# Optimization experiments

Hardware: AMD Instinct MI355X
Metric: run time of the kernel (lower is better)

Reference implementation:

```python
import jax, jax.numpy as jnp
import numpy as np

B, HW, ENC, E, D, A, V, L = 64, 14, 2048, 512, 512, 512, 32000, 32
LN_EPS = 1e-5


def setup_inputs() -> dict:
    key = jax.random.key(0)
    ks = jax.random.split(key, 16)
    s = 0.02
    n = lambda k, sh: jax.random.normal(k, sh, jnp.float32)
    encoder_out = n(ks[0], (B, HW, HW, ENC))
    encoded_captions = jax.random.randint(ks[1], (B, L), 0, V)
    caption_lengths = jax.random.randint(ks[2], (B, 1), 2, L + 1)
    caption_lengths = caption_lengths.at[0, 0].set(L)  # ensure max length present
    return dict(
        encoder_out=encoder_out,
        encoded_captions=encoded_captions,
        caption_lengths=caption_lengths,
        emb=n(ks[3], (V, E)) * s,
        W_enc_att=n(ks[4], (A, ENC)) * s, b_enc_att=jnp.zeros((A,)),
        W_dec_att=n(ks[5], (A, D)) * s, b_dec_att=jnp.zeros((A,)),
        W_full_att=n(ks[6], (1, A)) * s, b_full_att=jnp.zeros((1,)),
        W_ih=n(ks[7], (4 * D, E + ENC)) * s, b_ih=jnp.zeros((4 * D,)),
        W_hh=n(ks[8], (4 * D, D)) * s, b_hh=jnp.zeros((4 * D,)),
        g_h=jnp.ones((D,)), be_h=jnp.zeros((D,)),
        g_c=jnp.ones((D,)), be_c=jnp.zeros((D,)),
        W_init_h=n(ks[9], (D, ENC)) * s, b_init_h=jnp.zeros((D,)),
        W_init_c=n(ks[10], (D, ENC)) * s, b_init_c=jnp.zeros((D,)),
        W_beta=n(ks[11], (ENC, D)) * s, b_beta=jnp.zeros((ENC,)),
        W_fc=n(ks[12], (V, D)) * s, b_fc=jnp.zeros((V,)),
    )


def _layer_norm(x, g, b):
    m = x.mean(-1, keepdims=True)
    v = ((x - m) ** 2).mean(-1, keepdims=True)
    return (x - m) / jnp.sqrt(v + LN_EPS) * g + b


def reference(encoder_out, encoded_captions, caption_lengths, emb,
              W_enc_att, b_enc_att, W_dec_att, b_dec_att, W_full_att, b_full_att,
              W_ih, b_ih, W_hh, b_hh, g_h, be_h, g_c, be_c,
              W_init_h, b_init_h, W_init_c, b_init_c, W_beta, b_beta, W_fc, b_fc):
    bsz = encoder_out.shape[0]
    enc_out = encoder_out.reshape(bsz, -1, encoder_out.shape[-1])  # [B,P,ENC]
    lengths = caption_lengths[:, 0]
    order = jnp.argsort(-lengths)  # stable descending sort (matches torch sort)
    lengths = lengths[order]
    enc_out = enc_out[order]
    caps = encoded_captions[order]
    embeds = emb[caps]  # [B,L,E]
    decode_lengths = lengths - 1
    T = caps.shape[1] - 1  # static max(decode_lengths)

    mean_enc = enc_out.mean(axis=1)
    h = _layer_norm(mean_enc @ W_init_h.T + b_init_h, g_h, be_h)
    c = _layer_norm(mean_enc @ W_init_c.T + b_init_c, g_c, be_c)

    att1 = enc_out @ W_enc_att.T + b_enc_att  # [B,P,A] precomputed once
    prev_seq = jnp.swapaxes(embeds[:, :T], 0, 1)  # [T,B,E] teacher-forced inputs
    masks = jnp.arange(T)[:, None] < decode_lengths[None, :]  # [T,B] active rows

    def step(carry, xs):
        h, c = carry
        prev, mask = xs
        # attention
        att2 = h @ W_dec_att.T + b_dec_att  # [B,A]
        e = jax.nn.relu(att1 + att2[:, None, :]) @ W_full_att[0] + b_full_att[0]  # [B,P]
        alpha = jax.nn.softmax(e, axis=1)
        awe = jnp.einsum('bpe,bp->be', enc_out, alpha)  # [B,ENC]
        gate = jax.nn.sigmoid(h @ W_beta.T + b_beta)
        awe = gate * awe
        # LSTM cell
        x = jnp.concatenate([prev, awe], axis=1)  # [B,E+ENC]
        gates = x @ W_ih.T + b_ih + h @ W_hh.T + b_hh
        i, f, g, o = jnp.split(gates, 4, axis=1)
        c_new = jax.nn.sigmoid(f) * c + jax.nn.sigmoid(i) * jnp.tanh(g)
        h_new = jax.nn.sigmoid(o) * jnp.tanh(c_new)
        h_new = _layer_norm(h_new, g_h, be_h)
        c_new = _layer_norm(c_new, g_c, be_c)
        preds = h_new @ W_fc.T + b_fc  # [B,V]; dropout is identity in eval
        m = mask[:, None]
        h = jnp.where(m, h_new, h)  # freeze finished rows (== torch batch shrink)
        c = jnp.where(m, c_new, c)
        return (h, c), (jnp.where(m, preds, 0.0), jnp.where(m, alpha, 0.0))

    (_, _), (preds_t, alphas_t) = jax.lax.scan(step, (h, c), (prev_seq, masks))
    predictions = jnp.swapaxes(preds_t, 0, 1)  # [B,T,V]
    alphas = jnp.swapaxes(alphas_t, 0, 1)      # [B,T,P]
    return predictions, caps, decode_lengths, alphas, order
```

## Files before the change

### kernel.cpp

```cpp
#include <hip/hip_runtime.h>
#include <cfloat>
#include <math.h>

#define B_ 64
#define P_ 196
#define ENC_ 2048
#define D_ 512
#define V_ 32000
#define L_ 32
#define T_ 31

#define OUT_PREDS 0L
#define OUT_CAPS  63488000L
#define OUT_DECL  63490048L
#define OUT_ALPH  63490112L
#define OUT_ORDER 63878976L

typedef __bf16 bf16;
typedef __bf16 bf16x8 __attribute__((ext_vector_type(8)));
typedef __bf16 bf16x4 __attribute__((ext_vector_type(4)));
typedef __bf16 bf16x2 __attribute__((ext_vector_type(2)));
typedef float  f32x4  __attribute__((ext_vector_type(4)));

static __device__ __forceinline__ float sigmoidf_(float x) { return 1.f / (1.f + __expf(-x)); }

__global__ void k_order(const int* __restrict__ cap_len, const int* __restrict__ caps,
                        int* __restrict__ order_i, int* __restrict__ declen_i,
                        int* __restrict__ caps_i, float* __restrict__ out)
{
    __shared__ int len_s[B_];
    int tid = threadIdx.x;
    len_s[tid] = cap_len[tid];
    __syncthreads();
    int li = len_s[tid];
    int pos = 0;
    for (int j = 0; j < B_; ++j) {
        int lj = len_s[j];
        pos += (lj > li) || (lj == li && j < tid);
    }
    order_i[pos]  = tid;
    declen_i[pos] = li - 1;
    out[OUT_ORDER + pos] = (float)tid;
    out[OUT_DECL  + pos] = (float)(li - 1);
    for (int l = 0; l < L_; ++l) {
        int tok = caps[tid * L_ + l];
        caps_i[pos * L_ + l] = tok;
        out[OUT_CAPS + pos * L_ + l] = (float)tok;
    }
}

__global__ __launch_bounds__(256) void k_cvt(const float* __restrict__ in, bf16* __restrict__ ob, long n)
{
    long i = ((long)blockIdx.x * 256 + threadIdx.x) * 8;
    if (i >= n) return;
    float4 a = *(const float4*)(in + i);
    float4 b = *(const float4*)(in + i + 4);
    bf16x8 v;
    v[0]=(bf16)a.x; v[1]=(bf16)a.y; v[2]=(bf16)a.z; v[3]=(bf16)a.w;
    v[4]=(bf16)b.x; v[5]=(bf16)b.y; v[6]=(bf16)b.z; v[7]=(bf16)b.w;
    *(bf16x8*)(ob + i) = v;
}

__global__ __launch_bounds__(256) void k_cvt_enc(const float* __restrict__ enc,
                                                 const int* __restrict__ order_i,
                                                 bf16* __restrict__ enc_s)
{
    long i = ((long)blockIdx.x * 256 + threadIdx.x) * 8;
    int b = (int)(i / ((long)P_ * ENC_));
    long rem = i - (long)b * P_ * ENC_;
    const float* src = enc + (long)order_i[b] * P_ * ENC_ + rem;
    float4 a = *(const float4*)(src);
    float4 c = *(const float4*)(src + 4);
    bf16x8 v;
    v[0]=(bf16)a.x; v[1]=(bf16)a.y; v[2]=(bf16)a.z; v[3]=(bf16)a.w;
    v[4]=(bf16)c.x; v[5]=(bf16)c.y; v[6]=(bf16)c.z; v[7]=(bf16)c.w;
    *(bf16x8*)(enc_s + i) = v;
}

__global__ __launch_bounds__(256) void k_meanb(const bf16* __restrict__ enc_s, bf16* __restrict__ mean_b)
{
    int b = blockIdx.x, col = blockIdx.y * 256 + threadIdx.x;
    float s = 0.f;
    const bf16* eb = enc_s + (long)b * P_ * ENC_ + col;
    for (int p = 0; p < P_; ++p) s += (float)eb[(long)p * ENC_];
    mean_b[(long)b * ENC_ + col] = (bf16)(s * (1.f / (float)P_));
}

template<int FUSE, int EPI, int SWZ>
__global__ void __launch_bounds__(256)
k_mgemm(const bf16* __restrict__ A, long lda,
        const bf16* __restrict__ B1, const bf16* __restrict__ B2,
        const float* __restrict__ bias,
        float* __restrict__ Cf, bf16* __restrict__ Cb,
        int N, int K, int kspl, int Nsp, int Ksp,
        const int* __restrict__ declen_i)
{
    const int tid = threadIdx.x;
    const int lane = tid & 63, w = tid >> 6;
    int mt, nt, z;
    if (SWZ == 0)      { mt = blockIdx.x; nt = blockIdx.y; z = blockIdx.z; }
    else if (SWZ == 1) { int o = blockIdx.x; int wg = (o & 7) * 98 + (o >> 3);
                         mt = wg >> 2; nt = wg & 3; z = 0; }
    else               { int o = blockIdx.x; int xcd = o & 7;
                         int base = xcd < 6 ? xcd * 969 : 5814 + (xcd - 6) * 968;
                         int wg = base + (o >> 3);
                         nt = wg / 31; mt = wg - 31 * nt; z = 0; }
    const int krange = K / kspl;
    const int k0 = z * krange, k1 = k0 + krange;
    const int r16 = lane & 15, kq = lane >> 4;
    const int koff = kq * 8;

    const bf16* Ap = A + (long)(mt * 64 + r16) * lda + koff;
    const int ncol0 = nt * 128 + w * 32;

    const bf16* Bp[2];
    const bf16* B2p[2];
#pragma unroll
    for (int ni = 0; ni < 2; ++ni) {
        int n = ncol0 + ni * 16 + r16;
        if (FUSE == 1)
            Bp[ni] = (n < Nsp) ? B1 + (long)n * K + koff
                               : B2 + (long)(n - Nsp) * K + koff;
        else if (FUSE == 2) {
            Bp[ni]  = B1 + (long)n * Ksp + koff;
            B2p[ni] = B2 + (long)n * (K - Ksp) + koff - Ksp;
        } else
            Bp[ni] = B1 + (long)n * K + koff;
    }

    auto loadA = [&](int kk, bf16x8* dst) {
#pragma unroll
        for (int mi = 0; mi < 4; ++mi)
            dst[mi] = *(const bf16x8*)(Ap + (long)mi * 16 * lda + kk);
    };
    auto loadB = [&](int kk, bf16x8* dst) {
#pragma unroll
        for (int ni = 0; ni < 2; ++ni) {
            if (FUSE == 2 && kk >= Ksp) dst[ni] = *(const bf16x8*)(B2p[ni] + kk);
            else                        dst[ni] = *(const bf16x8*)(Bp[ni] + kk);
        }
    };

    f32x4 acc[4][2] = {};
    bf16x8 af[4], bfr[2];
    loadA(k0, af); loadB(k0, bfr);
    for (int kk = k0 + 32; kk < k1; kk += 32) {
        bf16x8 af2[4], bf2[2];
        loadA(kk, af2); loadB(kk, bf2);
#pragma unroll
        for (int mi = 0; mi < 4; ++mi)
#pragma unroll
            for (int ni = 0; ni < 2; ++ni)
                acc[mi][ni] = __builtin_amdgcn_mfma_f32_16x16x32_bf16(bfr[ni], af[mi], acc[mi][ni], 0, 0, 0);
#pragma unroll
        for (int mi = 0; mi < 4; ++mi) af[mi] = af2[mi];
#pragma unroll
        for (int ni = 0; ni < 2; ++ni) bfr[ni] = bf2[ni];
    }
#pragma unroll
    for (int mi = 0; mi < 4; ++mi)
#pragma unroll
        for (int ni = 0; ni < 2; ++ni)
            acc[mi][ni] = __builtin_amdgcn_mfma_f32_16x16x32_bf16(bfr[ni], af[mi], acc[mi][ni], 0, 0, 0);

#pragma unroll
    for (int mi = 0; mi < 4; ++mi) {
        const int row = mt * 64 + mi * 16 + r16;
#pragma unroll
        for (int ni = 0; ni < 2; ++ni) {
            const int col = ncol0 + ni * 16 + kq * 4;
            f32x4 v = acc[mi][ni];
            if (EPI == 0) {
                *(f32x4*)(Cf + (long)z * 64 * N + (long)row * N + col) = v;
            } else if (EPI == 1) {
                f32x4 bv = *(const f32x4*)(bias + col);
                bf16x4 o;
                o[0]=(bf16)(v[0]+bv[0]); o[1]=(bf16)(v[1]+bv[1]);
                o[2]=(bf16)(v[2]+bv[2]); o[3]=(bf16)(v[3]+bv[3]);
                *(bf16x4*)(Cb + (long)row * N + col) = o;
            } else {
                int tt = row >> 6, b = row & 63;
                bool msk = tt < declen_i[b];
                f32x4 bv = *(const f32x4*)(bias + col);
                f32x4 o;
                o[0] = msk ? v[0]+bv[0] : 0.f; o[1] = msk ? v[1]+bv[1] : 0.f;
                o[2] = msk ? v[2]+bv[2] : 0.f; o[3] = msk ? v[3]+bv[3] : 0.f;
                *(f32x4*)(Cf + OUT_PREDS + ((long)b * T_ + tt) * V_ + col) = o;
            }
        }
    }
}

static __device__ __forceinline__ void ln_stats(float x, float* r1, float* r2,
                                                float& m, float& var)
{
    int tid = threadIdx.x;
    r1[tid] = x; r2[tid] = x * x;
    __syncthreads();
    for (int s = 256; s > 0; s >>= 1) {
        if (tid < s) { r1[tid] += r1[tid + s]; r2[tid] += r2[tid + s]; }
        __syncthreads();
    }
    m = r1[0] * (1.f / 512.f);
    var = r2[0] * (1.f / 512.f) - m * m;
    __syncthreads();
}

__global__ __launch_bounds__(512)
void k_initln(const float* __restrict__ pi,
              const float* __restrict__ b_h, const float* __restrict__ b_c,
              const float* __restrict__ g_h, const float* __restrict__ be_h,
              const float* __restrict__ g_c, const float* __restrict__ be_c,
              bf16* __restrict__ xh, float* __restrict__ c)
{
    int b = blockIdx.x, d = threadIdx.x;
    float yh = pi[(long)b * 1024 + d]       + b_h[d];
    float yc = pi[(long)b * 1024 + 512 + d] + b_c[d];
    __shared__ float r1[512], r2[512];
    float m, v;
    ln_stats(yh, r1, r2, m, v);
    xh[(long)b * 3072 + 2560 + d] = (bf16)((yh - m) * rsqrtf(v + 1e-5f) * g_h[d] + be_h[d]);
    ln_stats(yc, r1, r2, m, v);
    c[(long)b * 512 + d] = (yc - m) * rsqrtf(v + 1e-5f) * g_c[d] + be_c[d];
}

__global__ __launch_bounds__(256)
void k_alpha(const float* __restrict__ att2gate, const float* __restrict__ b_dec,
             const float* __restrict__ Wfull, const bf16* __restrict__ att1_b,
             const int* __restrict__ caps_i, const int* __restrict__ declen_i,
             const float* __restrict__ emb, float* __restrict__ alpha_b,
             bf16* __restrict__ xh, float* __restrict__ out, int t)
{
    const int b = blockIdx.x, tid = threadIdx.x;
    if (t >= declen_i[b]) {
        if (tid < P_) out[OUT_ALPH + ((long)b * T_ + t) * P_ + tid] = 0.f;
        return;
    }
    __shared__ float att2s[512], wf[512], red[256];
    for (int i = tid; i < 512; i += 256) {
        float s = b_dec[i];
#pragma unroll
        for (int zz = 0; zz < 4; ++zz) s += att2gate[((long)zz * 64 + b) * 2560 + i];
        att2s[i] = s;
        wf[i] = Wfull[i];
    }
    __syncthreads();
    float ev = -FLT_MAX;
    if (tid < P_) {
        const bf16* ar = att1_b + ((long)b * P_ + tid) * 512;
        float acc = 0.f;
        for (int a0 = 0; a0 < 512; a0 += 8) {
            bf16x8 v = *(const bf16x8*)(ar + a0);
#pragma unroll
            for (int j = 0; j < 8; ++j)
                acc += fmaxf((float)v[j] + att2s[a0 + j], 0.f) * wf[a0 + j];
        }
        ev = acc;
    }
    red[tid] = ev;
    __syncthreads();
    for (int s = 128; s > 0; s >>= 1) { if (tid < s) red[tid] = fmaxf(red[tid], red[tid + s]); __syncthreads(); }
    float mx = red[0];
    __syncthreads();
    float ex = (tid < P_) ? __expf(ev - mx) : 0.f;
    red[tid] = ex;
    __syncthreads();
    for (int s = 128; s > 0; s >>= 1) { if (tid < s) red[tid] += red[tid + s]; __syncthreads(); }
    float inv = 1.f / red[0];
    if (tid < P_) {
        float al = ex * inv;
        alpha_b[b * P_ + tid] = al;
        out[OUT_ALPH + ((long)b * T_ + t) * P_ + tid] = al;
    }
    int tok = caps_i[b * L_ + t];
    for (int i = tid; i < 512; i += 256)
        xh[(long)b * 3072 + i] = (bf16)emb[(long)tok * 512 + i];
}

__global__ __launch_bounds__(256)
void k_awe(const float* __restrict__ alpha_b, const float* __restrict__ att2gate,
           const float* __restrict__ b_beta, const bf16* __restrict__ enc_s,
           const int* __restrict__ declen_i, bf16* __restrict__ xh, int t)
{
    const int b = blockIdx.x, tid = threadIdx.x;
    if (t >= declen_i[b]) return;
    __shared__ float alp[P_];
    if (tid < P_) alp[tid] = alpha_b[b * P_ + tid];
    __syncthreads();
    const int col = blockIdx.y * 512 + tid * 2;
    const bf16* eb = enc_s + (long)b * P_ * ENC_ + col;
    float a0 = 0.f, a1 = 0.f;
#pragma unroll 4
    for (int p = 0; p < P_; ++p) {
        bf16x2 v = *(const bf16x2*)(eb + (long)p * ENC_);
        float al = alp[p];
        a0 += al * (float)v[0]; a1 += al * (float)v[1];
    }
    float g0 = b_beta[col], g1 = b_beta[col + 1];
#pragma unroll
    for (int zz = 0; zz < 4; ++zz) {
        const float* gs = att2gate + ((long)zz * 64 + b) * 2560 + 512 + col;
        g0 += gs[0]; g1 += gs[1];
    }
    bf16x2 o;
    o[0] = (bf16)(a0 * sigmoidf_(g0));
    o[1] = (bf16)(a1 * sigmoidf_(g1));
    *(bf16x2*)(xh + (long)b * 3072 + 512 + col) = o;
}

__global__ __launch_bounds__(512)
void k_lstm(const float* __restrict__ gp, const float* __restrict__ b_ih, const float* __restrict__ b_hh,
            const float* __restrict__ g_h, const float* __restrict__ be_h,
            const float* __restrict__ g_c, const float* __restrict__ be_c,
            bf16* __restrict__ xh, float* __restrict__ c, bf16* __restrict__ hseq,
            const int* __restrict__ declen_i, int t)
{
    int b = blockIdx.x, d = threadIdx.x;
    if (t >= declen_i[b]) return;
    float iv = b_ih[d]        + b_hh[d];
    float fv = b_ih[512 + d]  + b_hh[512 + d];
    float gv = b_ih[1024 + d] + b_hh[1024 + d];
    float ov = b_ih[1536 + d] + b_hh[1536 + d];
    for (int s = 0; s < 8; ++s) {
        const float* gs = gp + ((long)s * B_ + b) * 2048;
        iv += gs[d]; fv += gs[512 + d]; gv += gs[1024 + d]; ov += gs[1536 + d];
    }
    float cn = sigmoidf_(fv) * c[(long)b * 512 + d] + sigmoidf_(iv) * tanhf(gv);
    float hn = sigmoidf_(ov) * tanhf(cn);
    __shared__ float r1[512], r2[512];
    float m, v;
    ln_stats(hn, r1, r2, m, v);
    float hln = (hn - m) * rsqrtf(v + 1e-5f) * g_h[d] + be_h[d];
    ln_stats(cn, r1, r2, m, v);
    float cln = (cn - m) * rsqrtf(v + 1e-5f) * g_c[d] + be_c[d];
    bf16 hv = (bf16)hln;
    xh[(long)b * 3072 + 2560 + d] = hv;
    hseq[((long)t * B_ + b) * 512 + d] = hv;
    c[(long)b * 512 + d] = cln;
}

extern "C" void kernel_launch(void* const* d_in, const int* in_sizes, int n_in,
                              void* d_out, int out_size, void* d_ws, size_t ws_size,
                              hipStream_t stream)
{
    const float* enc       = (const float*)d_in[0];
    const int*   caps      = (const int*)  d_in[1];
    const int*   caplen    = (const int*)  d_in[2];
    const float* emb       = (const float*)d_in[3];
    const float* W_enc_att = (const float*)d_in[4];
    const float* b_enc_att = (const float*)d_in[5];
    const float* W_dec_att = (const float*)d_in[6];
    const float* b_dec_att = (const float*)d_in[7];
    const float* W_full    = (const float*)d_in[8];
    const float* W_ih      = (const float*)d_in[10];
    const float* b_ih      = (const float*)d_in[11];
    const float* W_hh      = (const float*)d_in[12];
    const float* b_hh      = (const float*)d_in[13];
    const float* g_h       = (const float*)d_in[14];
    const float* be_h      = (const float*)d_in[15];
    const float* g_c       = (const float*)d_in[16];
    const float* be_c      = (const float*)d_in[17];
    const float* W_init_h  = (const float*)d_in[18];
    const float* b_init_h  = (const float*)d_in[19];
    const float* W_init_c  = (const float*)d_in[20];
    const float* b_init_c  = (const float*)d_in[21];
    const float* W_beta    = (const float*)d_in[22];
    const float* b_beta    = (const float*)d_in[23];
    const float* W_fc      = (const float*)d_in[24];
    const float* b_fc      = (const float*)d_in[25];
    float* out = (float*)d_out;

    char* w = (char*)d_ws;
    auto alloc = [&](size_t bytes) { char* p = w; w += (bytes + 255) & ~(size_t)255; return p; };
    int*   order_i  = (int*)  alloc(B_ * 4);
    int*   declen_i = (int*)  alloc(B_ * 4);
    int*   caps_i   = (int*)  alloc(B_ * L_ * 4);
    bf16*  enc_s    = (bf16*) alloc((size_t)B_ * P_ * ENC_ * 2);
    bf16*  mean_b   = (bf16*) alloc((size_t)B_ * ENC_ * 2);
    bf16*  att1_b   = (bf16*) alloc((size_t)B_ * P_ * 512 * 2);
    float* pi       = (float*)alloc((size_t)B_ * 1024 * 4);
    float* att2gate = (float*)alloc((size_t)4 * B_ * 2560 * 4);
    float* alpha_b  = (float*)alloc((size_t)B_ * P_ * 4);
    bf16*  xh       = (bf16*) alloc((size_t)B_ * 3072 * 2);
    float* gp       = (float*)alloc((size_t)8 * B_ * 2048 * 4);
    float* cbuf     = (float*)alloc((size_t)B_ * 512 * 4);
    bf16*  hseq     = (bf16*) alloc((size_t)T_ * B_ * 512 * 2);
    bf16*  W_enc_b  = (bf16*) alloc((size_t)512 * 2048 * 2);
    bf16*  W_dec_b  = (bf16*) alloc((size_t)512 * 512 * 2);
    bf16*  W_beta_b = (bf16*) alloc((size_t)2048 * 512 * 2);
    bf16*  W_ih_b   = (bf16*) alloc((size_t)2048 * 2560 * 2);
    bf16*  W_hh_b   = (bf16*) alloc((size_t)2048 * 512 * 2);
    bf16*  W_fc_b   = (bf16*) alloc((size_t)32000 * 512 * 2);
    bf16*  W_inh_b  = (bf16*) alloc((size_t)512 * 2048 * 2);
    bf16*  W_inc_b  = (bf16*) alloc((size_t)512 * 2048 * 2);

    k_order<<<1, B_, 0, stream>>>(caplen, caps, order_i, declen_i, caps_i, out);
    k_cvt_enc<<<12544, 256, 0, stream>>>(enc, order_i, enc_s);
    k_meanb<<<dim3(B_, 8), 256, 0, stream>>>(enc_s, mean_b);

    auto cvt = [&](const float* src, bf16* dst, long n) {
        k_cvt<<<(int)((n / 8 + 255) / 256), 256, 0, stream>>>(src, dst, n);
    };
    cvt(W_enc_att, W_enc_b, 512L * 2048);
    cvt(W_dec_att, W_dec_b, 512L * 512);
    cvt(W_beta,    W_beta_b, 2048L * 512);
    cvt(W_ih,      W_ih_b,  2048L * 2560);
    cvt(W_hh,      W_hh_b,  2048L * 512);
    cvt(W_fc,      W_fc_b,  32000L * 512);
    cvt(W_init_h,  W_inh_b, 512L * 2048);
    cvt(W_init_c,  W_inc_b, 512L * 2048);

    k_mgemm<1, 0, 0><<<dim3(1, 8, 1), 256, 0, stream>>>(mean_b, 2048, W_inh_b, W_inc_b,
        nullptr, pi, nullptr, 1024, 2048, 1, 512, 0, nullptr);
    k_initln<<<B_, 512, 0, stream>>>(pi, b_init_h, b_init_c, g_h, be_h, g_c, be_c, xh, cbuf);

    k_mgemm<0, 1, 1><<<784, 256, 0, stream>>>(enc_s, 2048, W_enc_b, nullptr,
        b_enc_att, nullptr, att1_b, 512, 2048, 1, 0, 0, nullptr);

    for (int t = 0; t < T_; ++t) {
        k_mgemm<1, 0, 0><<<dim3(1, 20, 4), 256, 0, stream>>>(xh + 2560, 3072, W_dec_b, W_beta_b,
            nullptr, att2gate, nullptr, 2560, 512, 4, 512, 0, nullptr);
        k_alpha<<<B_, 256, 0, stream>>>(att2gate, b_dec_att, W_full, att1_b,
            caps_i, declen_i, emb, alpha_b, xh, out, t);
        k_awe<<<dim3(B_, 4), 256, 0, stream>>>(alpha_b, att2gate, b_beta, enc_s,
            declen_i, xh, t);
        k_mgemm<2, 0, 0><<<dim3(1, 16, 8), 256, 0, stream>>>(xh, 3072, W_ih_b, W_hh_b,
            nullptr, gp, nullptr, 2048, 3072, 8, 0, 2560, nullptr);
        k_lstm<<<B_, 512, 0, stream>>>(gp, b_ih, b_hh, g_h, be_h, g_c, be_c,
            xh, cbuf, hseq, declen_i, t);
    }

    k_mgemm<0, 2, 2><<<7750, 256, 0, stream>>>(hseq, 512, W_fc_b, nullptr,
        b_fc, out, nullptr, V_, 512, 1, 0, 0, declen_i);
}
```

Before: 2.516 ms.

## Fuse per-timestep decoder kernels into one persistent kernel with grid barriers

Replaces the 31×5 per-timestep kernel launches (attention GEMM, alpha, awe, LSTM GEMM, LSTM cell) with a single persistent kernel of 256 blocks that loops over timesteps and separates phases with a software global barrier built on atomics. The attention-weighted encoding is now computed by 4 blocks per batch row, and each of those blocks recomputes the softmax redundantly so alpha no longer goes through global memory. The aim is to remove launch overhead and inter-kernel gaps on the serial recurrence. In exchange it relies on all 256 blocks being co-resident and spinning, and each phase leaves many blocks idle.

```diff
diff --git a/kernel.cpp b/kernel.cpp
--- a/kernel.cpp
+++ b/kernel.cpp
@@ -9,6 +9,7 @@
 #define V_ 32000
 #define L_ 32
 #define T_ 31
+#define NBLK_ 256
 
 #define OUT_PREDS 0L
 #define OUT_CAPS  63488000L
@@ -26,10 +27,12 @@
 
 __global__ void k_order(const int* __restrict__ cap_len, const int* __restrict__ caps,
                         int* __restrict__ order_i, int* __restrict__ declen_i,
-                        int* __restrict__ caps_i, float* __restrict__ out)
+                        int* __restrict__ caps_i, float* __restrict__ out,
+                        unsigned* __restrict__ bar)
 {
     __shared__ int len_s[B_];
     int tid = threadIdx.x;
+    if (tid == 0) { bar[0] = 0u; bar[1] = 0u; }
     len_s[tid] = cap_len[tid];
     __syncthreads();
     int li = len_s[tid];
@@ -92,7 +95,7 @@
         const bf16* __restrict__ B1, const bf16* __restrict__ B2,
         const float* __restrict__ bias,
         float* __restrict__ Cf, bf16* __restrict__ Cb,
-        int N, int K, int kspl, int Nsp, int Ksp,
+        int N, int K, int kspl, int Nsp,
         const int* __restrict__ declen_i)
 {
     const int tid = threadIdx.x;
@@ -114,39 +117,28 @@
     const int ncol0 = nt * 128 + w * 32;
 
     const bf16* Bp[2];
-    const bf16* B2p[2];
 #pragma unroll
     for (int ni = 0; ni < 2; ++ni) {
         int n = ncol0 + ni * 16 + r16;
         if (FUSE == 1)
             Bp[ni] = (n < Nsp) ? B1 + (long)n * K + koff
                                : B2 + (long)(n - Nsp) * K + koff;
-        else if (FUSE == 2) {
-            Bp[ni]  = B1 + (long)n * Ksp + koff;
-            B2p[ni] = B2 + (long)n * (K - Ksp) + koff - Ksp;
-        } else
+        else
             Bp[ni] = B1 + (long)n * K + koff;
     }
-
-    auto loadA = [&](int kk, bf16x8* dst) {
-#pragma unroll
-        for (int mi = 0; mi < 4; ++mi)
-            dst[mi] = *(const bf16x8*)(Ap + (long)mi * 16 * lda + kk);
-    };
-    auto loadB = [&](int kk, bf16x8* dst) {
-#pragma unroll
-        for (int ni = 0; ni < 2; ++ni) {
-            if (FUSE == 2 && kk >= Ksp) dst[ni] = *(const bf16x8*)(B2p[ni] + kk);
-            else                        dst[ni] = *(const bf16x8*)(Bp[ni] + kk);
-        }
-    };
 
     f32x4 acc[4][2] = {};
     bf16x8 af[4], bfr[2];
-    loadA(k0, af); loadB(k0, bfr);
+#pragma unroll
+    for (int mi = 0; mi < 4; ++mi) af[mi] = *(const bf16x8*)(Ap + (long)mi * 16 * lda + k0);
+#pragma unroll
+    for (int ni = 0; ni < 2; ++ni) bfr[ni] = *(const bf16x8*)(Bp[ni] + k0);
     for (int kk = k0 + 32; kk < k1; kk += 32) {
         bf16x8 af2[4], bf2[2];
-        loadA(kk, af2); loadB(kk, bf2);
+#pragma unroll
+        for (int mi = 0; mi < 4; ++mi) af2[mi] = *(const bf16x8*)(Ap + (long)mi * 16 * lda + kk);
+#pragma unroll
+        for (int ni = 0; ni < 2; ++ni) bf2[ni] = *(const bf16x8*)(Bp[ni] + kk);
 #pragma unroll
         for (int mi = 0; mi < 4; ++mi)
 #pragma unroll
@@ -224,119 +216,234 @@
     c[(long)b * 512 + d] = (yc - m) * rsqrtf(v + 1e-5f) * g_c[d] + be_c[d];
 }
 
+static __device__ __forceinline__ void gbar(unsigned* bar)
+{
+    __threadfence();
+    __syncthreads();
+    if (threadIdx.x == 0) {
+        unsigned g = __hip_atomic_load(&bar[1], __ATOMIC_RELAXED, __HIP_MEMORY_SCOPE_AGENT);
+        unsigned a = __hip_atomic_fetch_add(&bar[0], 1u, __ATOMIC_ACQ_REL, __HIP_MEMORY_SCOPE_AGENT);
+        if (a == (unsigned)(NBLK_ - 1)) {
+            __hip_atomic_store(&bar[0], 0u, __ATOMIC_RELAXED, __HIP_MEMORY_SCOPE_AGENT);
+            __hip_atomic_store(&bar[1], g + 1u, __ATOMIC_RELEASE, __HIP_MEMORY_SCOPE_AGENT);
+        } else {
+            while (__hip_atomic_load(&bar[1], __ATOMIC_RELAXED, __HIP_MEMORY_SCOPE_AGENT) == g)
+                __builtin_amdgcn_s_sleep(1);
+        }
+    }
+    __syncthreads();
+    __threadfence();
+}
+
 __global__ __launch_bounds__(256)
-void k_alpha(const float* __restrict__ att2gate, const float* __restrict__ b_dec,
-             const float* __restrict__ Wfull, const bf16* __restrict__ att1_b,
+void k_steps(const bf16* __restrict__ att1_b, const bf16* __restrict__ enc_s,
+             const bf16* __restrict__ Wd,  const bf16* __restrict__ Wbt,
+             const bf16* __restrict__ Wih, const bf16* __restrict__ Whh,
+             const float* __restrict__ b_dec, const float* __restrict__ b_beta,
+             const float* __restrict__ Wfull,
+             const float* __restrict__ b_ih, const float* __restrict__ b_hh,
+             const float* __restrict__ g_h, const float* __restrict__ be_h,
+             const float* __restrict__ g_c, const float* __restrict__ be_c,
              const int* __restrict__ caps_i, const int* __restrict__ declen_i,
-             const float* __restrict__ emb, float* __restrict__ alpha_b,
-             bf16* __restrict__ xh, float* __restrict__ out, int t)
-{
-    const int b = blockIdx.x, tid = threadIdx.x;
-    if (t >= declen_i[b]) {
-        if (tid < P_) out[OUT_ALPH + ((long)b * T_ + t) * P_ + tid] = 0.f;
-        return;
-    }
-    __shared__ float att2s[512], wf[512], red[256];
-    for (int i = tid; i < 512; i += 256) {
-        float s = b_dec[i];
-#pragma unroll
-        for (int zz = 0; zz < 4; ++zz) s += att2gate[((long)zz * 64 + b) * 2560 + i];
-        att2s[i] = s;
-        wf[i] = Wfull[i];
-    }
-    __syncthreads();
-    float ev = -FLT_MAX;
-    if (tid < P_) {
-        const bf16* ar = att1_b + ((long)b * P_ + tid) * 512;
-        float acc = 0.f;
-        for (int a0 = 0; a0 < 512; a0 += 8) {
-            bf16x8 v = *(const bf16x8*)(ar + a0);
-#pragma unroll
-            for (int j = 0; j < 8; ++j)
-                acc += fmaxf((float)v[j] + att2s[a0 + j], 0.f) * wf[a0 + j];
+             const float* __restrict__ emb,
+             bf16* __restrict__ xh, float* __restrict__ cst,
+             float* __restrict__ att2gate, float* __restrict__ gp,
+             bf16* __restrict__ hseq, float* __restrict__ out,
+             unsigned* __restrict__ bar)
+{
+    const int bid = blockIdx.x, tid = threadIdx.x;
+    const int lane = tid & 63, w = tid >> 6;
+    const int r16 = lane & 15, kq = lane >> 4, koff = kq * 8;
+    __shared__ float att2s[512], wf[512], red[256], alp[P_];
+    __shared__ float r1[256], r2[256];
+
+    for (int t = 0; t < T_; ++t) {
+        if (bid < 80) {
+            const int nt = bid % 20, z = bid / 20;
+            const int k0 = z * 128;
+            const int ncol0 = nt * 128 + w * 32;
+            const bf16* Ap = xh + 2560 + (long)r16 * 3072 + koff;
+            const bf16* Bp[2];
+#pragma unroll
+            for (int ni = 0; ni < 2; ++ni) {
+                int n = ncol0 + ni * 16 + r16;
+                Bp[ni] = ((n < 512) ? Wd + (long)n * 512 : Wbt + (long)(n - 512) * 512) + koff;
+            }
+            f32x4 acc[4][2] = {};
+#pragma unroll
+            for (int kk = k0; kk < k0 + 128; kk += 32) {
+                bf16x8 af[4], bfr[2];
+#pragma unroll
+                for (int mi = 0; mi < 4; ++mi) af[mi] = *(const bf16x8*)(Ap + (long)mi * 16 * 3072 + kk);
+#pragma unroll
+                for (int ni = 0; ni < 2; ++ni) bfr[ni] = *(const bf16x8*)(Bp[ni] + kk);
+#pragma unroll
+                for (int mi = 0; mi < 4; ++mi)
+#pragma unroll
+                    for (int ni = 0; ni < 2; ++ni)
+                        acc[mi][ni] = __builtin_amdgcn_mfma_f32_16x16x32_bf16(bfr[ni], af[mi], acc[mi][ni], 0, 0, 0);
+            }
+            float* C = att2gate + (long)z * 64 * 2560;
+#pragma unroll
+            for (int mi = 0; mi < 4; ++mi) {
+                const int row = mi * 16 + r16;
+#pragma unroll
+                for (int ni = 0; ni < 2; ++ni)
+                    *(f32x4*)(C + (long)row * 2560 + ncol0 + ni * 16 + kq * 4) = acc[mi][ni];
+            }
         }
-        ev = acc;
-    }
-    red[tid] = ev;
-    __syncthreads();
-    for (int s = 128; s > 0; s >>= 1) { if (tid < s) red[tid] = fmaxf(red[tid], red[tid + s]); __syncthreads(); }
-    float mx = red[0];
-    __syncthreads();
-    float ex = (tid < P_) ? __expf(ev - mx) : 0.f;
-    red[tid] = ex;
-    __syncthreads();
-    for (int s = 128; s > 0; s >>= 1) { if (tid < s) red[tid] += red[tid + s]; __syncthreads(); }
-    float inv = 1.f / red[0];
-    if (tid < P_) {
-        float al = ex * inv;
-        alpha_b[b * P_ + tid] = al;
-        out[OUT_ALPH + ((long)b * T_ + t) * P_ + tid] = al;
-    }
-    int tok = caps_i[b * L_ + t];
-    for (int i = tid; i < 512; i += 256)
-        xh[(long)b * 3072 + i] = (bf16)emb[(long)tok * 512 + i];
-}
-
-__global__ __launch_bounds__(256)
-void k_awe(const float* __restrict__ alpha_b, const float* __restrict__ att2gate,
-           const float* __restrict__ b_beta, const bf16* __restrict__ enc_s,
-           const int* __restrict__ declen_i, bf16* __restrict__ xh, int t)
-{
-    const int b = blockIdx.x, tid = threadIdx.x;
-    if (t >= declen_i[b]) return;
-    __shared__ float alp[P_];
-    if (tid < P_) alp[tid] = alpha_b[b * P_ + tid];
-    __syncthreads();
-    const int col = blockIdx.y * 512 + tid * 2;
-    const bf16* eb = enc_s + (long)b * P_ * ENC_ + col;
-    float a0 = 0.f, a1 = 0.f;
+        gbar(bar);
+
+        {
+            const int b = bid >> 2, seg = bid & 3;
+            if (t < declen_i[b]) {
+                for (int i = tid; i < 512; i += 256) {
+                    float s = b_dec[i];
+#pragma unroll
+                    for (int z = 0; z < 4; ++z) s += att2gate[((long)z * 64 + b) * 2560 + i];
+                    att2s[i] = s;
+                    wf[i] = Wfull[i];
+                }
+                __syncthreads();
+                float ev = -FLT_MAX;
+                if (tid < P_) {
+                    const bf16* ar = att1_b + ((long)b * P_ + tid) * 512;
+                    float acc = 0.f;
+                    for (int a0 = 0; a0 < 512; a0 += 8) {
+                        bf16x8 v = *(const bf16x8*)(ar + a0);
+#pragma unroll
+                        for (int j = 0; j < 8; ++j)
+                            acc += fmaxf((float)v[j] + att2s[a0 + j], 0.f) * wf[a0 + j];
+                    }
+                    ev = acc;
+                }
+                red[tid] = ev;
+                __syncthreads();
+                for (int s = 128; s > 0; s >>= 1) { if (tid < s) red[tid] = fmaxf(red[tid], red[tid + s]); __syncthreads(); }
+                float mx = red[0];
+                __syncthreads();
+                float ex = (tid < P_) ? __expf(ev - mx) : 0.f;
+                red[tid] = ex;
+                __syncthreads();
+                for (int s = 128; s > 0; s >>= 1) { if (tid < s) red[tid] += red[tid + s]; __syncthreads(); }
+                float inv = 1.f / red[0];
+                if (tid < P_) alp[tid] = ex * inv;
+                __syncthreads();
+                if (seg == 1 && tid < P_)
+                    out[OUT_ALPH + ((long)b * T_ + t) * P_ + tid] = alp[tid];
+                const int c0 = seg * 512 + tid * 2;
+                const bf16* eb = enc_s + (long)b * P_ * ENC_ + c0;
+                float a0 = 0.f, a1 = 0.f;
 #pragma unroll 4
-    for (int p = 0; p < P_; ++p) {
-        bf16x2 v = *(const bf16x2*)(eb + (long)p * ENC_);
-        float al = alp[p];
-        a0 += al * (float)v[0]; a1 += al * (float)v[1];
-    }
-    float g0 = b_beta[col], g1 = b_beta[col + 1];
-#pragma unroll
-    for (int zz = 0; zz < 4; ++zz) {
-        const float* gs = att2gate + ((long)zz * 64 + b) * 2560 + 512 + col;
-        g0 += gs[0]; g1 += gs[1];
-    }
-    bf16x2 o;
-    o[0] = (bf16)(a0 * sigmoidf_(g0));
-    o[1] = (bf16)(a1 * sigmoidf_(g1));
-    *(bf16x2*)(xh + (long)b * 3072 + 512 + col) = o;
-}
-
-__global__ __launch_bounds__(512)
-void k_lstm(const float* __restrict__ gp, const float* __restrict__ b_ih, const float* __restrict__ b_hh,
-            const float* __restrict__ g_h, const float* __restrict__ be_h,
-            const float* __restrict__ g_c, const float* __restrict__ be_c,
-            bf16* __restrict__ xh, float* __restrict__ c, bf16* __restrict__ hseq,
-            const int* __restrict__ declen_i, int t)
-{
-    int b = blockIdx.x, d = threadIdx.x;
-    if (t >= declen_i[b]) return;
-    float iv = b_ih[d]        + b_hh[d];
-    float fv = b_ih[512 + d]  + b_hh[512 + d];
-    float gv = b_ih[1024 + d] + b_hh[1024 + d];
-    float ov = b_ih[1536 + d] + b_hh[1536 + d];
-    for (int s = 0; s < 8; ++s) {
-        const float* gs = gp + ((long)s * B_ + b) * 2048;
-        iv += gs[d]; fv += gs[512 + d]; gv += gs[1024 + d]; ov += gs[1536 + d];
-    }
-    float cn = sigmoidf_(fv) * c[(long)b * 512 + d] + sigmoidf_(iv) * tanhf(gv);
-    float hn = sigmoidf_(ov) * tanhf(cn);
-    __shared__ float r1[512], r2[512];
-    float m, v;
-    ln_stats(hn, r1, r2, m, v);
-    float hln = (hn - m) * rsqrtf(v + 1e-5f) * g_h[d] + be_h[d];
-    ln_stats(cn, r1, r2, m, v);
-    float cln = (cn - m) * rsqrtf(v + 1e-5f) * g_c[d] + be_c[d];
-    bf16 hv = (bf16)hln;
-    xh[(long)b * 3072 + 2560 + d] = hv;
-    hseq[((long)t * B_ + b) * 512 + d] = hv;
-    c[(long)b * 512 + d] = cln;
+                for (int p = 0; p < P_; ++p) {
+                    bf16x2 v = *(const bf16x2*)(eb + (long)p * ENC_);
+                    float al = alp[p];
+                    a0 += al * (float)v[0]; a1 += al * (float)v[1];
+                }
+                float g0 = b_beta[c0], g1 = b_beta[c0 + 1];
+#pragma unroll
+                for (int z = 0; z < 4; ++z) {
+                    const float* gs = att2gate + ((long)z * 64 + b) * 2560 + 512 + c0;
+                    g0 += gs[0]; g1 += gs[1];
+                }
+                bf16x2 o;
+                o[0] = (bf16)(a0 * sigmoidf_(g0));
+                o[1] = (bf16)(a1 * sigmoidf_(g1));
+                *(bf16x2*)(xh + (long)b * 3072 + 512 + c0) = o;
+                if (seg == 0) {
+                    int tok = caps_i[b * L_ + t];
+                    for (int i = tid; i < 512; i += 256)
+                        xh[(long)b * 3072 + i] = (bf16)emb[(long)tok * 512 + i];
+                }
+            } else {
+                if (seg == 1 && tid < P_)
+                    out[OUT_ALPH + ((long)b * T_ + t) * P_ + tid] = 0.f;
+            }
+        }
+        gbar(bar);
+
+        if (bid < 128) {
+            const int nt = bid & 15, z = bid >> 4;
+            const int k0 = z * 384;
+            const int ncol0 = nt * 128 + w * 32;
+            const bf16* Ap = xh + (long)r16 * 3072 + koff;
+            const bf16* Bih[2]; const bf16* Bhh[2];
+#pragma unroll
+            for (int ni = 0; ni < 2; ++ni) {
+                int n = ncol0 + ni * 16 + r16;
+                Bih[ni] = Wih + (long)n * 2560 + koff;
+                Bhh[ni] = Whh + (long)n * 512 + koff - 2560;
+            }
+            f32x4 acc[4][2] = {};
+            for (int kk = k0; kk < k0 + 384; kk += 32) {
+                bf16x8 af[4], bfr[2];
+#pragma unroll
+                for (int mi = 0; mi < 4; ++mi) af[mi] = *(const bf16x8*)(Ap + (long)mi * 16 * 3072 + kk);
+#pragma unroll
+                for (int ni = 0; ni < 2; ++ni)
+                    bfr[ni] = *(const bf16x8*)(((kk < 2560) ? Bih[ni] : Bhh[ni]) + kk);
+#pragma unroll
+                for (int mi = 0; mi < 4; ++mi)
+#pragma unroll
+                    for (int ni = 0; ni < 2; ++ni)
+                        acc[mi][ni] = __builtin_amdgcn_mfma_f32_16x16x32_bf16(bfr[ni], af[mi], acc[mi][ni], 0, 0, 0);
+            }
+            float* C = gp + (long)z * 64 * 2048;
+#pragma unroll
+            for (int mi = 0; mi < 4; ++mi) {
+                const int row = mi * 16 + r16;
+#pragma unroll
+                for (int ni = 0; ni < 2; ++ni)
+                    *(f32x4*)(C + (long)row * 2048 + ncol0 + ni * 16 + kq * 4) = acc[mi][ni];
+            }
+        }
+        gbar(bar);
+
+        if (bid < 64) {
+            const int b = bid;
+            if (t < declen_i[b]) {
+                const int d0 = tid, d1 = tid + 256;
+                float iv0 = b_ih[d0] + b_hh[d0],             iv1 = b_ih[d1] + b_hh[d1];
+                float fv0 = b_ih[512+d0] + b_hh[512+d0],     fv1 = b_ih[512+d1] + b_hh[512+d1];
+                float gv0 = b_ih[1024+d0] + b_hh[1024+d0],   gv1 = b_ih[1024+d1] + b_hh[1024+d1];
+                float ov0 = b_ih[1536+d0] + b_hh[1536+d0],   ov1 = b_ih[1536+d1] + b_hh[1536+d1];
+#pragma unroll
+                for (int z = 0; z < 8; ++z) {
+                    const float* gs = gp + ((long)z * 64 + b) * 2048;
+                    iv0 += gs[d0]; fv0 += gs[512+d0]; gv0 += gs[1024+d0]; ov0 += gs[1536+d0];
+                    iv1 += gs[d1]; fv1 += gs[512+d1]; gv1 += gs[1024+d1]; ov1 += gs[1536+d1];
+                }
+                float c0 = cst[(long)b * 512 + d0], c1 = cst[(long)b * 512 + d1];
+                float cn0 = sigmoidf_(fv0) * c0 + sigmoidf_(iv0) * tanhf(gv0);
+                float cn1 = sigmoidf_(fv1) * c1 + sigmoidf_(iv1) * tanhf(gv1);
+                float hn0 = sigmoidf_(ov0) * tanhf(cn0);
+                float hn1 = sigmoidf_(ov1) * tanhf(cn1);
+                r1[tid] = hn0 + hn1; r2[tid] = hn0*hn0 + hn1*hn1;
+                __syncthreads();
+                for (int s = 128; s > 0; s >>= 1) { if (tid < s) { r1[tid]+=r1[tid+s]; r2[tid]+=r2[tid+s]; } __syncthreads(); }
+                float m = r1[0] * (1.f/512.f), vv = r2[0] * (1.f/512.f) - m*m;
+                float rs = rsqrtf(vv + 1e-5f);
+                float hl0 = (hn0 - m) * rs * g_h[d0] + be_h[d0];
+                float hl1 = (hn1 - m) * rs * g_h[d1] + be_h[d1];
+                __syncthreads();
+                r1[tid] = cn0 + cn1; r2[tid] = cn0*cn0 + cn1*cn1;
+                __syncthreads();
+                for (int s = 128; s > 0; s >>= 1) { if (tid < s) { r1[tid]+=r1[tid+s]; r2[tid]+=r2[tid+s]; } __syncthreads(); }
+                float m2 = r1[0] * (1.f/512.f), vv2 = r2[0] * (1.f/512.f) - m2*m2;
+                float rs2 = rsqrtf(vv2 + 1e-5f);
+                float cl0 = (cn0 - m2) * rs2 * g_c[d0] + be_c[d0];
+                float cl1 = (cn1 - m2) * rs2 * g_c[d1] + be_c[d1];
+                bf16 hv0 = (bf16)hl0, hv1 = (bf16)hl1;
+                xh[(long)b * 3072 + 2560 + d0] = hv0;
+                xh[(long)b * 3072 + 2560 + d1] = hv1;
+                hseq[((long)t * B_ + b) * 512 + d0] = hv0;
+                hseq[((long)t * B_ + b) * 512 + d1] = hv1;
+                cst[(long)b * 512 + d0] = cl0;
+                cst[(long)b * 512 + d1] = cl1;
+            }
+        }
+        gbar(bar);
+    }
 }
 
 extern "C" void kernel_launch(void* const* d_in, const int* in_sizes, int n_in,
@@ -375,12 +482,12 @@
     int*   order_i  = (int*)  alloc(B_ * 4);
     int*   declen_i = (int*)  alloc(B_ * 4);
     int*   caps_i   = (int*)  alloc(B_ * L_ * 4);
+    unsigned* bar   = (unsigned*)alloc(256);
     bf16*  enc_s    = (bf16*) alloc((size_t)B_ * P_ * ENC_ * 2);
     bf16*  mean_b   = (bf16*) alloc((size_t)B_ * ENC_ * 2);
     bf16*  att1_b   = (bf16*) alloc((size_t)B_ * P_ * 512 * 2);
     float* pi       = (float*)alloc((size_t)B_ * 1024 * 4);
     float* att2gate = (float*)alloc((size_t)4 * B_ * 2560 * 4);
-    float* alpha_b  = (float*)alloc((size_t)B_ * P_ * 4);
     bf16*  xh       = (bf16*) alloc((size_t)B_ * 3072 * 2);
     float* gp       = (float*)alloc((size_t)8 * B_ * 2048 * 4);
     float* cbuf     = (float*)alloc((size_t)B_ * 512 * 4);
@@ -394,7 +501,7 @@
     bf16*  W_inh_b  = (bf16*) alloc((size_t)512 * 2048 * 2);
     bf16*  W_inc_b  = (bf16*) alloc((size_t)512 * 2048 * 2);
 
-    k_order<<<1, B_, 0, stream>>>(caplen, caps, order_i, declen_i, caps_i, out);
+    k_order<<<1, B_, 0, stream>>>(caplen, caps, order_i, declen_i, caps_i, out, bar);
     k_cvt_enc<<<12544, 256, 0, stream>>>(enc, order_i, enc_s);
     k_meanb<<<dim3(B_, 8), 256, 0, stream>>>(enc_s, mean_b);
 
@@ -411,25 +518,16 @@
     cvt(W_init_c,  W_inc_b, 512L * 2048);
 
     k_mgemm<1, 0, 0><<<dim3(1, 8, 1), 256, 0, stream>>>(mean_b, 2048, W_inh_b, W_inc_b,
-        nullptr, pi, nullptr, 1024, 2048, 1, 512, 0, nullptr);
+        nullptr, pi, nullptr, 1024, 2048, 1, 512, nullptr);
     k_initln<<<B_, 512, 0, stream>>>(pi, b_init_h, b_init_c, g_h, be_h, g_c, be_c, xh, cbuf);
 
     k_mgemm<0, 1, 1><<<784, 256, 0, stream>>>(enc_s, 2048, W_enc_b, nullptr,
-        b_enc_att, nullptr, att1_b, 512, 2048, 1, 0, 0, nullptr);
-
-    for (int t = 0; t < T_; ++t) {
-        k_mgemm<1, 0, 0><<<dim3(1, 20, 4), 256, 0, stream>>>(xh + 2560, 3072, W_dec_b, W_beta_b,
-            nullptr, att2gate, nullptr, 2560, 512, 4, 512, 0, nullptr);
-        k_alpha<<<B_, 256, 0, stream>>>(att2gate, b_dec_att, W_full, att1_b,
-            caps_i, declen_i, emb, alpha_b, xh, out, t);
-        k_awe<<<dim3(B_, 4), 256, 0, stream>>>(alpha_b, att2gate, b_beta, enc_s,
-            declen_i, xh, t);
-        k_mgemm<2, 0, 0><<<dim3(1, 16, 8), 256, 0, stream>>>(xh, 3072, W_ih_b, W_hh_b,
-            nullptr, gp, nullptr, 2048, 3072, 8, 0, 2560, nullptr);
-        k_lstm<<<B_, 512, 0, stream>>>(gp, b_ih, b_hh, g_h, be_h, g_c, be_c,
-            xh, cbuf, hseq, declen_i, t);
-    }
+        b_enc_att, nullptr, att1_b, 512, 2048, 1, 0, nullptr);
+
+    k_steps<<<NBLK_, 256, 0, stream>>>(att1_b, enc_s, W_dec_b, W_beta_b, W_ih_b, W_hh_b,
+        b_dec_att, b_beta, W_full, b_ih, b_hh, g_h, be_h, g_c, be_c,
+        caps_i, declen_i, emb, xh, cbuf, att2gate, gp, hseq, out, bar);
 
     k_mgemm<0, 2, 2><<<7750, 256, 0, stream>>>(hseq, 512, W_fc_b, nullptr,
-        b_fc, out, nullptr, V_, 512, 1, 0, 0, declen_i);
-}
+        b_fc, out, nullptr, V_, 512, 1, 0, declen_i);
+}
```

Result: slower. 8.942 ms (+255.4%).
